# Kernel tuning notes

Measured on AMD Instinct MI355X. Metric: run time of the kernel, lower is better.

The kernel has to match this reference:

```python
import jax, jax.numpy as jnp
import numpy as np

B = 1024
P = 8
D = 2048
NUM_IDS = 64
MARGIN = 0.3
EPS = 1e-12


def setup_inputs() -> dict:
    key = jax.random.key(0)
    k1, k2, k3 = jax.random.split(key, 3)
    feats = jax.random.normal(k1, (B, P * D), dtype=jnp.float32)
    labels = jax.random.randint(k2, (B,), 0, NUM_IDS, dtype=jnp.int64)
    subs = jax.random.randint(k3, (B,), 0, 2, dtype=jnp.int64)
    return {"feats": feats, "labels": labels, "subs": subs}


def reference(feats, labels, subs):
    b = feats.shape[0]
    f = feats.reshape(b, -1, D)  # [B, P, D]
    dt = f.dtype

    # Per-sample class centers via a single segment-mean pass
    # (equivalent to the original per-sample boolean-mask mean loop).
    seg_sum = jax.ops.segment_sum(f, labels, num_segments=NUM_IDS)  # [NUM_IDS, P, D]
    counts = jax.ops.segment_sum(jnp.ones((b,), dt), labels, num_segments=NUM_IDS)
    centers_by_id = seg_sum / jnp.maximum(counts, 1.0)[:, None, None]
    centers = centers_by_id[labels]  # [B, P, D]

    # dist_ap[i] = sum_p ||f[i,p] - center[i,p]||
    d_ap = jnp.sqrt(jnp.clip(jnp.sum((f - centers) ** 2, axis=-1), EPS, None)).sum(-1)  # [B]
    dist_ap = d_ap[:, None] + d_ap[None, :]  # [B, B]

    # pairwise_distance: dist_aa[i,j] = sum_p ||f[i,p] - f[j,p]||, via gemm trick
    sq = jnp.sum(f * f, axis=-1)  # [B, P]
    inner = jnp.einsum('ipd,jpd->ijp', f, f)  # [B, B, P]
    d2 = sq[:, None, :] + sq[None, :, :] - 2.0 * inner
    dist_aa = jnp.sqrt(jnp.clip(d2, EPS, None)).sum(-1)  # [B, B]

    # masked margin loss over negative (different-label) pairs
    mask = labels[:, None] != labels[None, :]  # [B, B] bool
    vals = jnp.clip(dist_ap - dist_aa + MARGIN, 0.0, None)
    maskf = mask.astype(dt)
    loss = jnp.sum(vals * maskf) / jnp.sum(maskf)
    return loss
```

## Files before the change

kernel.cpp:

```cpp
#include <hip/hip_runtime.h>
#include <hip/hip_bf16.h>

#define B_ 1024
#define P_ 8
#define D_ 2048
#define FD_ (P_ * D_)
#define NID 64
#define MARGIN_ 0.3f
#define EPS_ 1e-12f
#define NPAIRBLK (8 * 8 * 8)

typedef unsigned short u16;
typedef float float4_t __attribute__((ext_vector_type(4)));

#define AS1 __attribute__((address_space(1)))
#define AS3 __attribute__((address_space(3)))

__device__ __forceinline__ float bf2f(u16 v) {
    unsigned x = (unsigned)v << 16;
    float f;
    __builtin_memcpy(&f, &x, 4);
    return f;
}

__device__ __forceinline__ float coh_read(float* p) { return atomicAdd(p, 0.0f); }

static const size_t OFF_COUNTS = 0;
static const size_t OFF_OFFS   = 256;
static const size_t OFF_PERM   = 512;
static const size_t OFF_NEG    = 4608;
static const size_t OFF_DONE   = 4616;
static const size_t OFF_POS    = 8176;
static const size_t OFF_S      = 8192;
static const size_t OFF_SQ     = 40960;
static const size_t OFF_DAP    = 73728;
static const size_t OFF_FB     = 131072;
static const size_t OFF_PD     = OFF_FB + (size_t)B_ * FD_;

__global__ void k_prep(const float* __restrict__ feats, const int* __restrict__ labels,
                       unsigned char* __restrict__ fb, float* __restrict__ sq,
                       float* countsf, int* offs, int* perm, float* negcnt,
                       float* S, float* possum, int* done) {
    int tid = threadIdx.x;
    if (blockIdx.x < B_) {
        int i = blockIdx.x;
        int w = tid >> 6, lane = tid & 63;
        const float* frow = feats + (size_t)i * FD_;
        unsigned char* brow = fb + (size_t)i * FD_;
#pragma unroll
        for (int pp = 0; pp < 2; pp++) {
            int p = w * 2 + pp;
            int off = p * D_;
            float s2 = 0.f;
#pragma unroll
            for (int ch = 0; ch < 8; ch++) {
                int d = off + ch * 256 + lane * 4;
                float4 f = *(const float4*)(frow + d);
                int pk = __builtin_amdgcn_cvt_pk_fp8_f32(f.x, f.y, 0, false);
                pk = __builtin_amdgcn_cvt_pk_fp8_f32(f.z, f.w, pk, true);
                *(unsigned int*)(brow + d) = (unsigned int)pk;
                s2 += f.x * f.x + f.y * f.y + f.z * f.z + f.w * f.w;
            }
            for (int o = 32; o; o >>= 1) s2 += __shfl_down(s2, o, 64);
            if (lane == 0) sq[i * P_ + p] = s2;
        }
        return;
    }
    __shared__ int h[NID], o[NID], cur[NID];
    if (tid < NID) h[tid] = 0;
    __syncthreads();
    for (int i = tid; i < B_; i += 256) atomicAdd(&h[labels[i]], 1);
    __syncthreads();
    if (tid == 0) {
        int acc = 0;
        long long ss = 0;
        for (int c = 0; c < NID; c++) {
            o[c] = acc;
            acc += h[c];
            ss += (long long)h[c] * h[c];
        }
        *negcnt = (float)((long long)B_ * B_ - ss);
        *possum = 0.f;
        done[0] = 0;
        done[1] = 0;
    }
    __syncthreads();
    if (tid < NID) {
        countsf[tid] = (float)h[tid];
        offs[tid] = o[tid];
        cur[tid] = o[tid];
    }
    __syncthreads();
    for (int i = tid; i < B_; i += 256) {
        int pos = atomicAdd(&cur[labels[i]], 1);
        perm[pos] = i;
    }
    for (int i = tid; i < B_ * P_; i += 256) S[i] = 0.f;
}

__global__ __launch_bounds__(512, 4) void k_pairs(const unsigned char* __restrict__ fb,
                                                  const float* __restrict__ sq,
                                                  const int* __restrict__ labels,
                                                  float* __restrict__ S,
                                                  u16* __restrict__ pd,
                                                  const float* __restrict__ countsf,
                                                  const int* __restrict__ offs,
                                                  const int* __restrict__ perm,
                                                  float* __restrict__ dap,
                                                  int* __restrict__ done) {
    const int i0 = blockIdx.y * 128, j0 = blockIdx.x * 128;
    const int p = blockIdx.z;
    __shared__ __align__(16) unsigned char smem[65536];
    __shared__ float sqAs[128], sqBs[128];
    __shared__ int labA[128], labB[128];
    const int tid = threadIdx.x;
    const int lane = tid & 63, wid = tid >> 6;
    const int s = wid & 3, h = wid >> 2;
    if (tid < 128) {
        sqAs[tid] = sq[(i0 + tid) * 8 + p];
        labA[tid] = labels[i0 + tid];
    } else if (tid < 256) {
        int t = tid - 128;
        sqBs[t] = sq[(j0 + t) * 8 + p];
        labB[t] = labels[j0 + t];
    }

    const int wi = (s >> 1) * 64, wj = (s & 1) * 64;
    const int lhi = lane >> 4, llo = lane & 15;
    const int sl = llo & 7;
    const int lr = lane >> 3;
    const int lc = (lane & 7) ^ lr;

    unsigned char* const As = smem + h * 16384;
    unsigned char* const Bs = smem + 32768 + h * 16384;

    const size_t colbase = (size_t)p * D_ + (size_t)h * 1024 + (size_t)lc * 16;
    const unsigned char* gA[4];
    const unsigned char* gB[4];
    unsigned char* lA[4];
    unsigned char* lB[4];
#pragma unroll
    for (int inst = 0; inst < 4; inst++) {
        int r0 = s * 32 + inst * 8;
        gA[inst] = fb + (size_t)(i0 + r0 + lr) * FD_ + colbase;
        gB[inst] = fb + (size_t)(j0 + r0 + lr) * FD_ + colbase;
        lA[inst] = As + r0 * 128;
        lB[inst] = Bs + r0 * 128;
    }

    float4_t acc[4][4];
#pragma unroll
    for (int a = 0; a < 4; a++)
#pragma unroll
        for (int b = 0; b < 4; b++) acc[a][b] = (float4_t){0.f, 0.f, 0.f, 0.f};

    for (int kb = 0; kb < 8; kb++) {
        const int koff = kb * 128;
        __syncthreads();
#pragma unroll
        for (int inst = 0; inst < 4; inst++) {
            __builtin_amdgcn_global_load_lds((const AS1 void*)(gA[inst] + koff),
                                             (AS3 void*)lA[inst], 16, 0, 0);
            __builtin_amdgcn_global_load_lds((const AS1 void*)(gB[inst] + koff),
                                             (AS3 void*)lB[inst], 16, 0, 0);
        }
        __syncthreads();
#pragma unroll
        for (int ks = 0; ks < 4; ks++) {
            const int pcb = ((2 * ks + (lhi >> 1)) ^ sl) * 16 + (lhi & 1) * 8;
            long af[4], bf[4];
#pragma unroll
            for (int a = 0; a < 4; a++) {
                af[a] = *(const long*)(As + (wi + a * 16 + llo) * 128 + pcb);
                bf[a] = *(const long*)(Bs + (wj + a * 16 + llo) * 128 + pcb);
            }
#pragma unroll
            for (int a = 0; a < 4; a++)
#pragma unroll
                for (int b = 0; b < 4; b++)
                    acc[a][b] = __builtin_amdgcn_mfma_f32_16x16x32_fp8_fp8(
                        af[a], bf[b], acc[a][b], 0, 0, 0);
        }
    }
    __syncthreads();
    float* ep = (float*)smem;
    if (h == 1) {
#pragma unroll
        for (int a = 0; a < 4; a++)
#pragma unroll
            for (int b = 0; b < 4; b++)
                *(float4_t*)&ep[(((s * 4 + a) * 4 + b) * 64 + lane) * 4] = acc[a][b];
    }
    __syncthreads();
    if (h == 0) {
        u16* outp = pd + (size_t)p * B_ * B_;
        float rs[4][4];
#pragma unroll
        for (int a = 0; a < 4; a++)
#pragma unroll
            for (int r = 0; r < 4; r++) rs[a][r] = 0.f;
#pragma unroll
        for (int a = 0; a < 4; a++) {
            int la0 = labA[wi + a * 16 + lhi * 4 + 0];
            int la1 = labA[wi + a * 16 + lhi * 4 + 1];
            int la2 = labA[wi + a * 16 + lhi * 4 + 2];
            int la3 = labA[wi + a * 16 + lhi * 4 + 3];
#pragma unroll
            for (int b = 0; b < 4; b++) {
                float4_t o = *(const float4_t*)&ep[(((s * 4 + a) * 4 + b) * 64 + lane) * 4];
                int lb = labB[wj + b * 16 + llo];
                int jl = wj + b * 16 + llo;
#pragma unroll
                for (int r = 0; r < 4; r++) {
                    int il = wi + a * 16 + lhi * 4 + r;
                    float t = acc[a][b][r] + o[r];
                    float d2 = sqAs[il] + sqBs[jl] - 2.0f * t;
                    outp[(size_t)(i0 + il) * B_ + (j0 + jl)] =
                        __bfloat16_as_ushort(__float2bfloat16(sqrtf(fmaxf(d2, EPS_))));
                    int la = (r == 0) ? la0 : (r == 1) ? la1 : (r == 2) ? la2 : la3;
                    if (lb == la) rs[a][r] += t;
                }
            }
        }
#pragma unroll
        for (int a = 0; a < 4; a++)
#pragma unroll
            for (int r = 0; r < 4; r++) {
                float v = rs[a][r];
                v += __shfl_xor(v, 1, 64);
                v += __shfl_xor(v, 2, 64);
                v += __shfl_xor(v, 4, 64);
                v += __shfl_xor(v, 8, 64);
                if (llo == 0)
                    atomicAdd(&S[(size_t)(i0 + wi + a * 16 + lhi * 4 + r) * 8 + p], v);
            }
    }

    __syncthreads();
    int* lastFlag = (int*)smem;
    float* Tl = (float*)(smem + 64);
    float* cntl = (float*)(smem + 64 + 2048);
    if (tid == 0) {
        __threadfence();
        int v = atomicAdd(done, 1);
        lastFlag[0] = (v == NPAIRBLK - 1) ? 1 : 0;
    }
    __syncthreads();
    if (!lastFlag[0]) return;
    {
        int c = tid >> 3, pp = tid & 7;
        int cnt = (int)countsf[c];
        int off = offs[c];
        float t = 0.f;
#pragma unroll 4
        for (int m = 0; m < cnt; m++) {
            int idx = perm[off + m];
            t += coh_read(&S[(size_t)idx * 8 + pp]);
        }
        Tl[c * 8 + pp] = t;
        if (pp == 0) cntl[c] = fmaxf((float)cnt, 1.f);
    }
    __syncthreads();
    for (int i = tid; i < B_; i += 512) {
        int c = labels[i];
        float n = cntl[c];
        float inv = 1.f / n, inv2 = inv * inv;
        float dsum = 0.f;
#pragma unroll
        for (int pp = 0; pp < 8; pp++) {
            float Sv = coh_read(&S[(size_t)i * 8 + pp]);
            float d2 = sq[i * 8 + pp] - 2.f * inv * Sv + inv2 * Tl[c * 8 + pp];
            dsum += sqrtf(fmaxf(d2, EPS_));
        }
        dap[i] = dsum;
    }
}

__global__ void k_lossred(const u16* __restrict__ pd, const float* __restrict__ dap,
                          const int* __restrict__ labels, float* possum,
                          const float* __restrict__ negcnt, int* __restrict__ done,
                          float* __restrict__ out) {
    int i = blockIdx.x;
    int tid = threadIdx.x;
    float di = dap[i];
    int li = labels[i];
    int j0 = tid * 4;
    float d0 = 0.f, d1 = 0.f, d2 = 0.f, d3 = 0.f;
#pragma unroll
    for (int p = 0; p < P_; p++) {
        ushort4 v = *(const ushort4*)&pd[(size_t)p * B_ * B_ + (size_t)i * B_ + j0];
        d0 += bf2f(v.x);
        d1 += bf2f(v.y);
        d2 += bf2f(v.z);
        d3 += bf2f(v.w);
    }
    int4 lj = *(const int4*)&labels[j0];
    float4 dj = *(const float4*)&dap[j0];
    float lsum = 0.f;
    if (lj.x != li) lsum += fmaxf(di + dj.x - d0 + MARGIN_, 0.f);
    if (lj.y != li) lsum += fmaxf(di + dj.y - d1 + MARGIN_, 0.f);
    if (lj.z != li) lsum += fmaxf(di + dj.z - d2 + MARGIN_, 0.f);
    if (lj.w != li) lsum += fmaxf(di + dj.w - d3 + MARGIN_, 0.f);
    for (int o = 32; o; o >>= 1) lsum += __shfl_down(lsum, o, 64);
    __shared__ float red[4];
    int wid = tid >> 6, lane = tid & 63;
    if (lane == 0) red[wid] = lsum;
    __syncthreads();
    if (tid == 0) {
        atomicAdd(possum, red[0] + red[1] + red[2] + red[3]);
        __threadfence();
        int v = atomicAdd(done, 1);
        if (v == B_ - 1) {
            float ps = atomicAdd(possum, 0.f);
            out[0] = ps / negcnt[0];
        }
    }
}

extern "C" void kernel_launch(void* const* d_in, const int* in_sizes, int n_in,
                              void* d_out, int out_size, void* d_ws, size_t ws_size,
                              hipStream_t stream) {
    const float* feats = (const float*)d_in[0];
    const int* labels  = (const int*)d_in[1];
    float* out = (float*)d_out;

    char* w = (char*)d_ws;
    float* countsf = (float*)(w + OFF_COUNTS);
    int* offs      = (int*)(w + OFF_OFFS);
    int* perm      = (int*)(w + OFF_PERM);
    float* negcnt  = (float*)(w + OFF_NEG);
    int* done      = (int*)(w + OFF_DONE);
    float* possum  = (float*)(w + OFF_POS);
    float* S       = (float*)(w + OFF_S);
    float* sq      = (float*)(w + OFF_SQ);
    float* dap     = (float*)(w + OFF_DAP);
    unsigned char* fb = (unsigned char*)(w + OFF_FB);
    u16* pd        = (u16*)(w + OFF_PD);

    k_prep<<<B_ + 1, 256, 0, stream>>>(feats, labels, fb, sq, countsf, offs, perm,
                                       negcnt, S, possum, done);
    k_pairs<<<dim3(8, 8, 8), 512, 0, stream>>>(fb, sq, labels, S, pd, countsf, offs,
                                               perm, dap, done);
    k_lossred<<<B_, 256, 0, stream>>>(pd, dap, labels, possum, negcnt, done + 1, out);
}
```

Baseline: 183.3 us.

## Split pair epilogue across both wave halves and move dist_ap tail into separate kernel

```diff
diff --git a/kernel.cpp b/kernel.cpp
--- a/kernel.cpp
+++ b/kernel.cpp
@@ -8,7 +8,6 @@
 #define NID 64
 #define MARGIN_ 0.3f
 #define EPS_ 1e-12f
-#define NPAIRBLK (8 * 8 * 8)
 
 typedef unsigned short u16;
 typedef float float4_t __attribute__((ext_vector_type(4)));
@@ -22,8 +21,6 @@
     __builtin_memcpy(&f, &x, 4);
     return f;
 }
-
-__device__ __forceinline__ float coh_read(float* p) { return atomicAdd(p, 0.0f); }
 
 static const size_t OFF_COUNTS = 0;
 static const size_t OFF_OFFS   = 256;
@@ -82,7 +79,6 @@
         *negcnt = (float)((long long)B_ * B_ - ss);
         *possum = 0.f;
         done[0] = 0;
-        done[1] = 0;
     }
     __syncthreads();
     if (tid < NID) {
@@ -102,12 +98,7 @@
                                                   const float* __restrict__ sq,
                                                   const int* __restrict__ labels,
                                                   float* __restrict__ S,
-                                                  u16* __restrict__ pd,
-                                                  const float* __restrict__ countsf,
-                                                  const int* __restrict__ offs,
-                                                  const int* __restrict__ perm,
-                                                  float* __restrict__ dap,
-                                                  int* __restrict__ done) {
+                                                  u16* __restrict__ pd) {
     const int i0 = blockIdx.y * 128, j0 = blockIdx.x * 128;
     const int p = blockIdx.z;
     __shared__ __align__(16) unsigned char smem[65536];
@@ -184,23 +175,26 @@
     }
     __syncthreads();
     float* ep = (float*)smem;
-    if (h == 1) {
-#pragma unroll
-        for (int a = 0; a < 4; a++)
+#pragma unroll
+    for (int a = 0; a < 4; a++) {
+        if ((h == 1) ? (a < 2) : (a >= 2)) {
 #pragma unroll
             for (int b = 0; b < 4; b++)
                 *(float4_t*)&ep[(((s * 4 + a) * 4 + b) * 64 + lane) * 4] = acc[a][b];
-    }
-    __syncthreads();
-    if (h == 0) {
+        }
+    }
+    __syncthreads();
+    {
+        const int abase = (h == 0) ? 0 : 2;
         u16* outp = pd + (size_t)p * B_ * B_;
-        float rs[4][4];
-#pragma unroll
-        for (int a = 0; a < 4; a++)
-#pragma unroll
-            for (int r = 0; r < 4; r++) rs[a][r] = 0.f;
-#pragma unroll
-        for (int a = 0; a < 4; a++) {
+        float rs[2][4];
+#pragma unroll
+        for (int ai = 0; ai < 2; ai++)
+#pragma unroll
+            for (int r = 0; r < 4; r++) rs[ai][r] = 0.f;
+#pragma unroll
+        for (int ai = 0; ai < 2; ai++) {
+            const int a = abase + ai;
             int la0 = labA[wi + a * 16 + lhi * 4 + 0];
             int la1 = labA[wi + a * 16 + lhi * 4 + 1];
             int la2 = labA[wi + a * 16 + lhi * 4 + 2];
@@ -218,61 +212,50 @@
                     outp[(size_t)(i0 + il) * B_ + (j0 + jl)] =
                         __bfloat16_as_ushort(__float2bfloat16(sqrtf(fmaxf(d2, EPS_))));
                     int la = (r == 0) ? la0 : (r == 1) ? la1 : (r == 2) ? la2 : la3;
-                    if (lb == la) rs[a][r] += t;
+                    if (lb == la) rs[ai][r] += t;
                 }
             }
         }
 #pragma unroll
-        for (int a = 0; a < 4; a++)
+        for (int ai = 0; ai < 2; ai++)
 #pragma unroll
             for (int r = 0; r < 4; r++) {
-                float v = rs[a][r];
+                float v = rs[ai][r];
                 v += __shfl_xor(v, 1, 64);
                 v += __shfl_xor(v, 2, 64);
                 v += __shfl_xor(v, 4, 64);
                 v += __shfl_xor(v, 8, 64);
                 if (llo == 0)
-                    atomicAdd(&S[(size_t)(i0 + wi + a * 16 + lhi * 4 + r) * 8 + p], v);
+                    atomicAdd(&S[(size_t)(i0 + wi + (abase + ai) * 16 + lhi * 4 + r) * 8 + p], v);
             }
     }
-
-    __syncthreads();
-    int* lastFlag = (int*)smem;
-    float* Tl = (float*)(smem + 64);
-    float* cntl = (float*)(smem + 64 + 2048);
-    if (tid == 0) {
-        __threadfence();
-        int v = atomicAdd(done, 1);
-        lastFlag[0] = (v == NPAIRBLK - 1) ? 1 : 0;
-    }
-    __syncthreads();
-    if (!lastFlag[0]) return;
-    {
-        int c = tid >> 3, pp = tid & 7;
-        int cnt = (int)countsf[c];
-        int off = offs[c];
+}
+
+__global__ void k_dap(const float* __restrict__ S, const float* __restrict__ sq,
+                      const float* __restrict__ countsf, const int* __restrict__ offs,
+                      const int* __restrict__ perm, float* __restrict__ dap) {
+    int c = blockIdx.x;
+    int tid = threadIdx.x;
+    int cnt = (int)countsf[c];
+    int off = offs[c];
+    __shared__ float T[8];
+    if (tid < 8) {
         float t = 0.f;
-#pragma unroll 4
-        for (int m = 0; m < cnt; m++) {
-            int idx = perm[off + m];
-            t += coh_read(&S[(size_t)idx * 8 + pp]);
-        }
-        Tl[c * 8 + pp] = t;
-        if (pp == 0) cntl[c] = fmaxf((float)cnt, 1.f);
-    }
-    __syncthreads();
-    for (int i = tid; i < B_; i += 512) {
-        int c = labels[i];
-        float n = cntl[c];
-        float inv = 1.f / n, inv2 = inv * inv;
-        float dsum = 0.f;
-#pragma unroll
-        for (int pp = 0; pp < 8; pp++) {
-            float Sv = coh_read(&S[(size_t)i * 8 + pp]);
-            float d2 = sq[i * 8 + pp] - 2.f * inv * Sv + inv2 * Tl[c * 8 + pp];
-            dsum += sqrtf(fmaxf(d2, EPS_));
-        }
-        dap[i] = dsum;
+        for (int m = 0; m < cnt; m++) t += S[(size_t)perm[off + m] * 8 + tid];
+        T[tid] = t;
+    }
+    __syncthreads();
+    float n = fmaxf((float)cnt, 1.f);
+    float inv = 1.f / n, inv2 = inv * inv;
+    for (int m = tid; m < cnt; m += 64) {
+        int i = perm[off + m];
+        float d = 0.f;
+#pragma unroll
+        for (int p = 0; p < 8; p++) {
+            float d2 = sq[i * 8 + p] - 2.f * inv * S[(size_t)i * 8 + p] + inv2 * T[p];
+            d += sqrtf(fmaxf(d2, EPS_));
+        }
+        dap[i] = d;
     }
 }
 
@@ -339,7 +322,7 @@
 
     k_prep<<<B_ + 1, 256, 0, stream>>>(feats, labels, fb, sq, countsf, offs, perm,
                                        negcnt, S, possum, done);
-    k_pairs<<<dim3(8, 8, 8), 512, 0, stream>>>(fb, sq, labels, S, pd, countsf, offs,
-                                               perm, dap, done);
-    k_lossred<<<B_, 256, 0, stream>>>(pd, dap, labels, possum, negcnt, done + 1, out);
-}
+    k_pairs<<<dim3(8, 8, 8), 512, 0, stream>>>(fb, sq, labels, S, pd);
+    k_dap<<<NID, 64, 0, stream>>>(S, sq, countsf, offs, perm, dap);
+    k_lossred<<<B_, 256, 0, stream>>>(pd, dap, labels, possum, negcnt, done, out);
+}
```

New measurement: 246.4 us. 34.4% more time.
